# Kernel tuning notes

Hardware: AMD Instinct MI355X
Metric: run time of the kernel (lower is better)

## Reference

```python
import jax, jax.numpy as jnp
import numpy as np

DIM = 192
HEADS = 4
RED = 4  # DFRG reduction


def _conv1x1(x, w):
    # x: [b,c,h,w], w: [o,c] (1x1 conv, no bias)
    return jnp.einsum('bchw,oc->bohw', x, w)


def _dfrg(x, w_fc1, w_fc2, w_spatial):
    # channel gate (SE-style with avg+max pooling)
    avg = jnp.mean(x, axis=(2, 3), keepdims=True)          # [b,c,1,1]
    mx = jnp.max(x, axis=(2, 3), keepdims=True)            # [b,c,1,1]
    pool = jnp.concatenate([avg, mx], axis=1)              # [b,2c,1,1]
    sq = jax.nn.relu(_conv1x1(pool, w_fc1))                # [b,c/RED,1,1]
    channel_gate = jax.nn.sigmoid(_conv1x1(sq, w_fc2))     # [b,c,1,1]
    # spatial gate (7x7 conv over [mean_c, max_c])
    sp = jnp.concatenate([jnp.mean(x, axis=1, keepdims=True),
                          jnp.max(x, axis=1, keepdims=True)], axis=1)  # [b,2,h,w]
    sg = jax.lax.conv_general_dilated(
        sp, w_spatial, (1, 1), [(3, 3), (3, 3)],
        dimension_numbers=('NCHW', 'OIHW', 'NCHW'))
    spatial_gate = jax.nn.sigmoid(sg)                      # [b,1,h,w]
    return x * channel_gate * spatial_gate


def _forward(x, w_fc1, w_fc2, w_spatial, w_qkv, w_dw, w_proj, temperature):
    b, c, h, w = x.shape
    hd = c // HEADS
    x = _dfrg(x, w_fc1, w_fc2, w_spatial)
    # qkv 1x1 conv (out channels = 4c for elementwise gate) + depthwise 3x3
    qkv = _conv1x1(x, w_qkv)                               # [b,4c,h,w]
    qkv = jax.lax.conv_general_dilated(
        qkv, w_dw, (1, 1), [(1, 1), (1, 1)],
        dimension_numbers=('NCHW', 'OIHW', 'NCHW'),
        feature_group_count=4 * c)
    # channel order matches torch: [q (c), gate (c), k (c), v (c)]
    q, gate, k, v = jnp.split(qkv, [c, 2 * c, 3 * c], axis=1)
    heads = lambda t: t.reshape(b, HEADS, hd, h * w)       # b head c (h w)
    q, k, v, gate = heads(q), heads(k), heads(v), heads(gate)
    # L2-normalize over spatial axis (F.normalize, eps=1e-12)
    q = q / jnp.maximum(jnp.linalg.norm(q, axis=-1, keepdims=True), 1e-12)
    k = k / jnp.maximum(jnp.linalg.norm(k, axis=-1, keepdims=True), 1e-12)
    attn = jnp.einsum('bhcn,bhdn->bhcd', q, k) * temperature  # [b,H,hd,hd]
    attn = jax.nn.softmax(attn, axis=-1)
    out = jnp.einsum('bhcd,bhdn->bhcn', attn, v)
    out = out * jax.nn.sigmoid(gate)                       # elementwise gating
    out = out.reshape(b, c, h, w)
    return _conv1x1(out, w_proj)


def setup_inputs() -> dict:
    key = jax.random.key(0)
    ks = jax.random.split(key, 8)
    b, c, h, w = 8, DIM, 128, 128
    s = 0.02
    return {
        'x': jax.random.normal(ks[0], (b, c, h, w), jnp.float32),
        'w_fc1': jax.random.normal(ks[1], (c // RED, 2 * c), jnp.float32) * s,
        'w_fc2': jax.random.normal(ks[2], (c, c // RED), jnp.float32) * s,
        'w_spatial': jax.random.normal(ks[3], (1, 2, 7, 7), jnp.float32) * s,
        'w_qkv': jax.random.normal(ks[4], (4 * c, c), jnp.float32) * s,
        'w_dw': jax.random.normal(ks[5], (4 * c, 1, 3, 3), jnp.float32) * s,
        'w_proj': jax.random.normal(ks[6], (c, c), jnp.float32) * s,
        'temperature': jnp.ones((HEADS, 1, 1), jnp.float32),
    }


def reference(x, w_fc1, w_fc2, w_spatial, w_qkv, w_dw, w_proj, temperature):
    return _forward(x, w_fc1, w_fc2, w_spatial, w_qkv, w_dw, w_proj, temperature)
```

## Files before the change

### kernel.cpp

```cpp
#include <hip/hip_runtime.h>
#include <cstdint>
#include <type_traits>

typedef unsigned int u32;
typedef unsigned short u16;
typedef short v8s __attribute__((ext_vector_type(8)));
typedef float v4f __attribute__((ext_vector_type(4)));

#define B_ 8
#define C_ 192
#define HW_ 16384
#define C4_ 768

__device__ __forceinline__ float b2f(u16 u) {
  union { u32 i; float f; } v; v.i = ((u32)u) << 16; return v.f;
}
__device__ __forceinline__ u16 f2b(float f) {
  union { float f; u32 i; } v; v.f = f;
  u32 r = v.i + 0x7fffu + ((v.i >> 16) & 1u);
  return (u16)(r >> 16);
}
__device__ __forceinline__ void b2f2(u32 u, float& a, float& b) {
  union { u32 i; float f; } x, y;
  x.i = u << 16; y.i = u & 0xffff0000u;
  a = x.f; b = y.f;
}
__device__ __forceinline__ float lo16f(u32 u) {
  union { u32 i; float f; } x; x.i = u << 16; return x.f;
}
__device__ __forceinline__ float hi16f(u32 u) {
  union { u32 i; float f; } x; x.i = u & 0xffff0000u; return x.f;
}
__device__ __forceinline__ float sigm(float x) { return 1.f / (1.f + expf(-x)); }
__device__ __forceinline__ u32 pk2(u16 a, u16 b) { return (u32)a | ((u32)b << 16); }

__global__ __launch_bounds__(256) void k_f2b(const float* __restrict__ in, u16* __restrict__ out, int n) {
  int i = blockIdx.x * 256 + threadIdx.x;
  if (i < n) out[i] = f2b(in[i]);
}

__global__ __launch_bounds__(256) void k_channel_pool(const float* __restrict__ x,
                                                      float* __restrict__ avg, float* __restrict__ mx_) {
  int c = blockIdx.x, b = blockIdx.y, t = threadIdx.x;
  const float4* p = (const float4*)(x + (((size_t)b * C_ + c) << 14));
  float s = 0.f, m = -INFINITY;
  for (int i = t; i < 4096; i += 256) {
    float4 v = p[i];
    s += v.x + v.y + v.z + v.w;
    m = fmaxf(m, fmaxf(fmaxf(v.x, v.y), fmaxf(v.z, v.w)));
  }
  __shared__ float ss[256], sm[256];
  ss[t] = s; sm[t] = m; __syncthreads();
  for (int o = 128; o > 0; o >>= 1) {
    if (t < o) { ss[t] += ss[t + o]; sm[t] = fmaxf(sm[t], sm[t + o]); }
    __syncthreads();
  }
  if (t == 0) { avg[b * C_ + c] = ss[0] * (1.f / 16384.f); mx_[b * C_ + c] = sm[0]; }
}

__global__ __launch_bounds__(256) void k_channel_gate(const float* __restrict__ avg, const float* __restrict__ mx_,
                                                      const float* __restrict__ wfc1, const float* __restrict__ wfc2,
                                                      float* __restrict__ cgate) {
  int b = blockIdx.x, t = threadIdx.x;
  __shared__ float pool[384], sq[48];
  if (t < 192) { pool[t] = avg[b * C_ + t]; pool[192 + t] = mx_[b * C_ + t]; }
  __syncthreads();
  if (t < 48) {
    float s = 0.f;
    for (int k = 0; k < 384; ++k) s += wfc1[t * 384 + k] * pool[k];
    sq[t] = fmaxf(s, 0.f);
  }
  __syncthreads();
  if (t < 192) {
    float s = 0.f;
    for (int j = 0; j < 48; ++j) s += wfc2[t * 48 + j] * sq[j];
    cgate[b * C_ + t] = sigm(s);
  }
}

__global__ __launch_bounds__(256) void k_spatial_pool(const float* __restrict__ x, float* __restrict__ sp) {
  int b = blockIdx.y;
  int p4 = blockIdx.x * 256 + threadIdx.x;
  const float4* xb = (const float4*)(x + (((size_t)b * C_) << 14)) + p4;
  float4 s; s.x = s.y = s.z = s.w = 0.f;
  float4 m; m.x = m.y = m.z = m.w = -INFINITY;
#pragma unroll 4
  for (int c = 0; c < C_; ++c) {
    float4 v = xb[(size_t)c << 12];
    s.x += v.x; s.y += v.y; s.z += v.z; s.w += v.w;
    m.x = fmaxf(m.x, v.x); m.y = fmaxf(m.y, v.y);
    m.z = fmaxf(m.z, v.z); m.w = fmaxf(m.w, v.w);
  }
  float4 sm;
  sm.x = s.x * (1.f / 192.f); sm.y = s.y * (1.f / 192.f);
  sm.z = s.z * (1.f / 192.f); sm.w = s.w * (1.f / 192.f);
  *(float4*)(sp + (size_t)b * 32768 + p4 * 4) = sm;
  *(float4*)(sp + (size_t)b * 32768 + 16384 + p4 * 4) = m;
}

__global__ __launch_bounds__(256) void k_spatial_conv(const float* __restrict__ sp, const float* __restrict__ wsp,
                                                      float* __restrict__ sg) {
  int b = blockIdx.y;
  int p = blockIdx.x * 256 + threadIdx.x;
  int y = p >> 7, xx = p & 127;
  const float* s0 = sp + (size_t)b * 32768;
  float acc = 0.f;
  for (int ic = 0; ic < 2; ++ic)
    for (int ky = 0; ky < 7; ++ky) {
      int yy = y + ky - 3;
      if ((unsigned)yy >= 128u) continue;
      for (int kx = 0; kx < 7; ++kx) {
        int xp = xx + kx - 3;
        if ((unsigned)xp >= 128u) continue;
        acc += wsp[ic * 49 + ky * 7 + kx] * s0[ic * 16384 + yy * 128 + xp];
      }
    }
  sg[(size_t)b * 16384 + p] = sigm(acc);
}

__global__ __launch_bounds__(256) void k_gxT(const float* __restrict__ x, const float* __restrict__ cg,
                                             const float* __restrict__ sg, u16* __restrict__ gxT, int b0) {
  int zb = blockIdx.y, b = b0 + zb, t = threadIdx.x;
  int hw0 = blockIdx.x * 64;
  __shared__ alignas(16) u16 Ls[64][196];
  int l16 = t & 15, grp = t >> 4;
  int px0 = l16 * 4;
  float4 sg4 = *(const float4*)(sg + (size_t)b * 16384 + hw0 + px0);
#pragma unroll
  for (int it = 0; it < 12; ++it) {
    int c = it * 16 + grp;
    float cgv = cg[b * C_ + c];
    float4 v = *(const float4*)(x + (((size_t)b * C_ + c) << 14) + hw0 + px0);
    Ls[px0 + 0][c] = f2b(v.x * cgv * sg4.x);
    Ls[px0 + 1][c] = f2b(v.y * cgv * sg4.y);
    Ls[px0 + 2][c] = f2b(v.z * cgv * sg4.z);
    Ls[px0 + 3][c] = f2b(v.w * cgv * sg4.w);
  }
  __syncthreads();
  u32* out = (u32*)gxT;
  for (int r = 0; r < 24; ++r) {
    int ci = r * 256 + t;
    int row = ci / 96, col = ci - row * 96;
    u32 v = *(const u32*)&Ls[row][col * 2];
    out[((size_t)zb * HW_ + hw0 + row) * 96 + col] = v;
  }
}

template <int M, typename OutT>
__global__ __launch_bounds__(256) void gemm_bt(const u16* __restrict__ A, const u16* __restrict__ BT,
                                               OutT* __restrict__ C) {
  const int K = 192;
  int b = blockIdx.z;
  int n0 = blockIdx.x * 128, m0 = blockIdx.y * 128;
  const u16* Bb = BT + (size_t)b * HW_ * K;
  __shared__ alignas(16) u16 SMEM[2 * 128 * 104];
  u16 (*As)[104] = (u16(*)[104])SMEM;
  u16 (*Bs)[104] = (u16(*)[104])(SMEM + 128 * 104);
  int t = threadIdx.x;
  int wave = t >> 6, lane = t & 63, l16 = lane & 15, quad = lane >> 4;
  int wr = wave >> 1, wc = wave & 1;
  v4f acc[4][4] = {};
  for (int kc = 0; kc < K; kc += 64) {
#pragma unroll
    for (int r = 0; r < 4; ++r) {
      int ci = r * 256 + t;
      int row = ci >> 3, ks = (ci & 7) * 8;
      uint4 av; av.x = av.y = av.z = av.w = 0u;
      if (M >= 768 || m0 + row < M) av = *(const uint4*)(A + (size_t)(m0 + row) * K + kc + ks);
      *(uint4*)&As[row][ks] = av;
      uint4 bv = *(const uint4*)(Bb + (size_t)(n0 + row) * K + kc + ks);
      *(uint4*)&Bs[row][ks] = bv;
    }
    __syncthreads();
#pragma unroll
    for (int s = 0; s < 2; ++s) {
      v8s af[4], bf[4];
#pragma unroll
      for (int mt = 0; mt < 4; ++mt) af[mt] = *(const v8s*)&As[wr * 64 + mt * 16 + l16][s * 32 + quad * 8];
#pragma unroll
      for (int nt = 0; nt < 4; ++nt) bf[nt] = *(const v8s*)&Bs[wc * 64 + nt * 16 + l16][s * 32 + quad * 8];
#pragma unroll
      for (int mt = 0; mt < 4; ++mt)
#pragma unroll
        for (int nt = 0; nt < 4; ++nt)
          acc[mt][nt] = __builtin_amdgcn_mfma_f32_16x16x32_bf16(af[mt], bf[nt], acc[mt][nt], 0, 0, 0);
    }
    __syncthreads();
  }
  char* eb = (char*)SMEM + wave * 10240;
  if constexpr (std::is_same<OutT, u16>::value) {
#pragma unroll
    for (int mt = 0; mt < 4; ++mt)
#pragma unroll
      for (int nt = 0; nt < 4; ++nt)
#pragma unroll
        for (int r = 0; r < 4; ++r) {
          int rr = mt * 16 + quad * 4 + r;
          *(u16*)(eb + rr * 160 + (nt * 16 + l16) * 2) = f2b(acc[mt][nt][r]);
        }
#pragma unroll
    for (int it = 0; it < 8; ++it) {
      int rr = it * 8 + (lane >> 3);
      uint4 v = *(const uint4*)(eb + rr * 160 + (lane & 7) * 16);
      int gm = m0 + wr * 64 + rr;
      size_t off = ((size_t)b * M + gm) * (size_t)HW_ + n0 + wc * 64 + (lane & 7) * 8;
      *(uint4*)(C + off) = v;
    }
  } else {
#pragma unroll
    for (int half = 0; half < 2; ++half) {
#pragma unroll
      for (int mt = 0; mt < 2; ++mt)
#pragma unroll
        for (int nt = 0; nt < 4; ++nt)
#pragma unroll
          for (int r = 0; r < 4; ++r) {
            int rr = mt * 16 + quad * 4 + r;
            *(float*)(eb + rr * 272 + (nt * 16 + l16) * 4) = acc[half * 2 + mt][nt][r];
          }
#pragma unroll
      for (int it = 0; it < 8; ++it) {
        int rr = it * 4 + (lane >> 4);
        uint4 v = *(const uint4*)(eb + rr * 272 + (lane & 15) * 16);
        int gm = m0 + wr * 64 + half * 32 + rr;
        if (gm < M) {
          size_t off = ((size_t)b * M + gm) * (size_t)HW_ + n0 + wc * 64 + (lane & 15) * 4;
          *(uint4*)((float*)C + off) = v;
        }
      }
    }
  }
}

__global__ __launch_bounds__(256) void k_dw(const u16* __restrict__ in, const float* __restrict__ wdw,
                                            u16* __restrict__ out) {
  int oc = blockIdx.y;
  size_t base = ((size_t)(blockIdx.z * C4_ + oc)) << 14;
  int t = threadIdx.x;
  int rp = t >> 4;
  int xseg = t & 15;
  int y0 = blockIdx.x * 32 + rp * 2;
  int x0 = xseg * 8;
  const float* wd = wdw + oc * 9;
  float w0 = wd[0], w1 = wd[1], w2 = wd[2];
  float w3 = wd[3], w4 = wd[4], w5 = wd[5];
  float w6 = wd[6], w7 = wd[7], w8 = wd[8];

  float r[4][10];
#pragma unroll
  for (int ky = 0; ky < 4; ++ky) {
    int yy = y0 + ky - 1;
    uint4 v; v.x = v.y = v.z = v.w = 0u;
    if ((unsigned)yy < 128u) v = *(const uint4*)(in + base + ((size_t)yy << 7) + x0);
    b2f2(v.x, r[ky][1], r[ky][2]);
    b2f2(v.y, r[ky][3], r[ky][4]);
    b2f2(v.z, r[ky][5], r[ky][6]);
    b2f2(v.w, r[ky][7], r[ky][8]);
    u32 pw = (u32)__shfl_up((int)v.w, 1);
    u32 nx = (u32)__shfl_down((int)v.x, 1);
    r[ky][0] = (xseg == 0) ? 0.f : hi16f(pw);
    r[ky][9] = (xseg == 15) ? 0.f : lo16f(nx);
  }

#pragma unroll
  for (int oy = 0; oy < 2; ++oy) {
    float acc[8];
#pragma unroll
    for (int j = 0; j < 8; ++j) {
      acc[j] = w0 * r[oy][j]     + w1 * r[oy][j + 1]     + w2 * r[oy][j + 2]
             + w3 * r[oy + 1][j] + w4 * r[oy + 1][j + 1] + w5 * r[oy + 1][j + 2]
             + w6 * r[oy + 2][j] + w7 * r[oy + 2][j + 1] + w8 * r[oy + 2][j + 2];
    }
    uint4 o;
    o.x = pk2(f2b(acc[0]), f2b(acc[1]));
    o.y = pk2(f2b(acc[2]), f2b(acc[3]));
    o.z = pk2(f2b(acc[4]), f2b(acc[5]));
    o.w = pk2(f2b(acc[6]), f2b(acc[7]));
    *(uint4*)(out + base + (((size_t)(y0 + oy)) << 7) + x0) = o;
  }
}

__global__ __launch_bounds__(256) void k_rnorm(const u16* __restrict__ qkv, float* __restrict__ rqn,
                                               float* __restrict__ rkn, int b0) {
  int j = blockIdx.x, zb = blockIdx.y, b = b0 + zb, t = threadIdx.x;
  int ch = (j < 192) ? j : (384 + j - 192);
  const uint4* p = (const uint4*)(qkv + (((size_t)zb * C4_ + ch) << 14));
  float s = 0.f;
  for (int i = t; i < 2048; i += 256) {
    uint4 v = p[i];
    float a, c;
    b2f2(v.x, a, c); s += a * a + c * c;
    b2f2(v.y, a, c); s += a * a + c * c;
    b2f2(v.z, a, c); s += a * a + c * c;
    b2f2(v.w, a, c); s += a * a + c * c;
  }
  __shared__ float ss[256];
  ss[t] = s; __syncthreads();
  for (int o = 128; o > 0; o >>= 1) {
    if (t < o) ss[t] += ss[t + o];
    __syncthreads();
  }
  if (t == 0) {
    float r = 1.f / fmaxf(sqrtf(ss[0]), 1e-12f);
    if (j < 192) rqn[b * C_ + j] = r; else rkn[b * C_ + (j - 192)] = r;
  }
}

__global__ __launch_bounds__(256) void k_qk(const u16* __restrict__ qkv, float* __restrict__ Spart, int b0) {
  int split = blockIdx.x;
  int zb = blockIdx.y >> 2, h = blockIdx.y & 3;
  int bh = (b0 + zb) * 4 + h;
  int t = threadIdx.x, w = t >> 6, lane = t & 63, l16 = lane & 15, quad = lane >> 4;
  __shared__ union U {
    struct { alignas(16) u16 Qs[48][136]; alignas(16) u16 Ks[48][136]; } qk;
    float R[4][48][49];
  } Sh;
  const u16* qb = qkv + (((size_t)zb * C4_ + h * 48) << 14);
  const u16* kb = qkv + (((size_t)zb * C4_ + 384 + h * 48) << 14);
  v4f acc[3][3] = {};
  for (int chunk = 0; chunk < 8; ++chunk) {
    int nb = split * 1024 + chunk * 128;
#pragma unroll
    for (int r = 0; r < 3; ++r) {
      int ci = r * 256 + t;
      int row = ci >> 4, cs = (ci & 15) * 8;
      *(uint4*)&Sh.qk.Qs[row][cs] = *(const uint4*)(qb + ((size_t)row << 14) + nb + cs);
      *(uint4*)&Sh.qk.Ks[row][cs] = *(const uint4*)(kb + ((size_t)row << 14) + nb + cs);
    }
    __syncthreads();
    v8s qf[3], kf[3];
#pragma unroll
    for (int mt = 0; mt < 3; ++mt) qf[mt] = *(const v8s*)&Sh.qk.Qs[mt * 16 + l16][w * 32 + quad * 8];
#pragma unroll
    for (int nt = 0; nt < 3; ++nt) kf[nt] = *(const v8s*)&Sh.qk.Ks[nt * 16 + l16][w * 32 + quad * 8];
#pragma unroll
    for (int mt = 0; mt < 3; ++mt)
#pragma unroll
      for (int nt = 0; nt < 3; ++nt)
        acc[mt][nt] = __builtin_amdgcn_mfma_f32_16x16x32_bf16(qf[mt], kf[nt], acc[mt][nt], 0, 0, 0);
    __syncthreads();
  }
#pragma unroll
  for (int mt = 0; mt < 3; ++mt)
#pragma unroll
    for (int nt = 0; nt < 3; ++nt)
#pragma unroll
      for (int r = 0; r < 4; ++r)
        Sh.R[w][nt * 16 + l16][mt * 16 + quad * 4 + r] = acc[mt][nt][r];
  __syncthreads();
  float* out = Spart + ((size_t)split * 32 + bh) * 2304;
#pragma unroll
  for (int rr = 0; rr < 9; ++rr) {
    int e = rr * 256 + t;
    int c = e / 48, d = e - c * 48;
    out[e] = (Sh.R[0][d][c] + Sh.R[1][d][c]) + (Sh.R[2][d][c] + Sh.R[3][d][c]);
  }
}

__global__ __launch_bounds__(256) void k_softmax(const float* __restrict__ Spart, const float* __restrict__ rqn,
                                                 const float* __restrict__ rkn, const float* __restrict__ temp,
                                                 float* __restrict__ attn, int b0) {
  int bh = b0 * 4 + blockIdx.x;
  int b = bh >> 2, h = bh & 3, t = threadIdx.x;
  __shared__ float Sm[2304];
  float tv = temp[h];
  for (int r = 0; r < 9; ++r) {
    int e = r * 256 + t;
    float s = 0.f;
#pragma unroll
    for (int p = 0; p < 16; ++p) s += Spart[((size_t)p * 32 + bh) * 2304 + e];
    int c = e / 48, d = e - c * 48;
    Sm[e] = s * rqn[b * C_ + h * 48 + c] * rkn[b * C_ + h * 48 + d] * tv;
  }
  __syncthreads();
  if (t < 48) {
    float m = -INFINITY;
#pragma unroll
    for (int d = 0; d < 48; ++d) m = fmaxf(m, Sm[t * 48 + d]);
    float ex[48];
    float sum = 0.f;
#pragma unroll
    for (int d = 0; d < 48; ++d) { ex[d] = expf(Sm[t * 48 + d] - m); sum += ex[d]; }
    float inv = 1.f / sum;
#pragma unroll
    for (int d = 0; d < 48; ++d) attn[(size_t)bh * 2304 + t * 48 + d] = ex[d] * inv;
  }
}

__global__ __launch_bounds__(256) void k_av(const u16* __restrict__ qkv, const float* __restrict__ attn,
                                            u16* __restrict__ ogT, int b0) {
  int zb = blockIdx.y >> 2, h = blockIdx.y & 3;
  int bh = (b0 + zb) * 4 + h;
  int t = threadIdx.x;
  int n0 = blockIdx.x * 512;
  __shared__ alignas(16) u16 Vs[48][520];
  __shared__ alignas(16) float SlT[48][48];
  for (int r = 0; r < 9; ++r) {
    int e = r * 256 + t;
    int c = e / 48, d = e - c * 48;
    SlT[d][c] = attn[(size_t)bh * 2304 + e];
  }
  const u16* vb = qkv + (((size_t)zb * C4_ + 576 + h * 48) << 14);
  for (int r = 0; r < 12; ++r) {
    int ci = r * 256 + t;
    int row = ci >> 6, cs = (ci & 63) * 8;
    *(uint4*)&Vs[row][cs] = *(const uint4*)(vb + ((size_t)row << 14) + n0 + cs);
  }
  __syncthreads();
  int grp = t >> 6, nl = t & 63;
  int n = n0 + nl * 8;
  float acc[12][8] = {};
  for (int d = 0; d < 48; ++d) {
    uint4 vv = *(const uint4*)&Vs[d][nl * 8];
    float v[8];
    b2f2(vv.x, v[0], v[1]); b2f2(vv.y, v[2], v[3]);
    b2f2(vv.z, v[4], v[5]); b2f2(vv.w, v[6], v[7]);
    const float4* sr = (const float4*)&SlT[d][grp * 12];
    float4 sa = sr[0], sb = sr[1], sc = sr[2];
    float sv[12] = {sa.x, sa.y, sa.z, sa.w, sb.x, sb.y, sb.z, sb.w, sc.x, sc.y, sc.z, sc.w};
#pragma unroll
    for (int cc = 0; cc < 12; ++cc)
#pragma unroll
      for (int j = 0; j < 8; ++j) acc[cc][j] += sv[cc] * v[j];
  }
  const u16* gb = qkv + (((size_t)zb * C4_ + 192 + h * 48) << 14);
#pragma unroll
  for (int cc = 0; cc < 12; ++cc) {
    int c = grp * 12 + cc;
    uint4 g4 = *(const uint4*)(gb + ((size_t)c << 14) + n);
    float g[8];
    b2f2(g4.x, g[0], g[1]); b2f2(g4.y, g[2], g[3]);
    b2f2(g4.z, g[4], g[5]); b2f2(g4.w, g[6], g[7]);
#pragma unroll
    for (int j = 0; j < 8; ++j) acc[cc][j] *= sigm(g[j]);
  }
#pragma unroll
  for (int j = 0; j < 8; ++j) {
    u16 vals[12];
#pragma unroll
    for (int cc = 0; cc < 12; ++cc) vals[cc] = f2b(acc[cc][j]);
    u16* dst = ogT + ((size_t)zb * HW_ + n + j) * 192 + h * 48 + grp * 12;
    uint2* d2 = (uint2*)dst;
    uint2 w0, w1, w2;
    w0.x = pk2(vals[0], vals[1]);  w0.y = pk2(vals[2], vals[3]);
    w1.x = pk2(vals[4], vals[5]);  w1.y = pk2(vals[6], vals[7]);
    w2.x = pk2(vals[8], vals[9]);  w2.y = pk2(vals[10], vals[11]);
    d2[0] = w0; d2[1] = w1; d2[2] = w2;
  }
}

extern "C" void kernel_launch(void* const* d_in, const int* in_sizes, int n_in,
                              void* d_out, int out_size, void* d_ws, size_t ws_size,
                              hipStream_t stream) {
  const float* x     = (const float*)d_in[0];
  const float* wfc1  = (const float*)d_in[1];
  const float* wfc2  = (const float*)d_in[2];
  const float* wsp   = (const float*)d_in[3];
  const float* wqkv  = (const float*)d_in[4];
  const float* wdw   = (const float*)d_in[5];
  const float* wproj = (const float*)d_in[6];
  const float* temp  = (const float*)d_in[7];
  float* out = (float*)d_out;
  char* W = (char*)d_ws;

  constexpr size_t OFF_AVG   = 0;
  constexpr size_t OFF_MAX   = 8192;
  constexpr size_t OFF_CG    = 16384;
  constexpr size_t OFF_RQN   = 24576;
  constexpr size_t OFF_RKN   = 32768;
  constexpr size_t OFF_WQB   = 40960;
  constexpr size_t OFF_WPB   = OFF_WQB + 294912;
  constexpr size_t OFF_SP    = OFF_WPB + 73728;
  constexpr size_t OFF_SG    = OFF_SP + 1048576;
  constexpr size_t OFF_ATT   = OFF_SG + 524288;
  constexpr size_t OFF_SPART = OFF_ATT + 294912;
  constexpr size_t OFF_BIG   = OFF_SPART + 4718592;
  const size_t GXT_B = (size_t)HW_ * 192 * 2;
  const size_t QKV_B = (size_t)C4_ * HW_ * 2;

  float* avg   = (float*)(W + OFF_AVG);
  float* mx    = (float*)(W + OFF_MAX);
  float* cg    = (float*)(W + OFF_CG);
  float* rqn   = (float*)(W + OFF_RQN);
  float* rkn   = (float*)(W + OFF_RKN);
  u16*   wqb   = (u16*)(W + OFF_WQB);
  u16*   wpb   = (u16*)(W + OFF_WPB);
  float* sp    = (float*)(W + OFF_SP);
  float* sg    = (float*)(W + OFF_SG);
  float* attn  = (float*)(W + OFF_ATT);
  float* Spart = (float*)(W + OFF_SPART);

  int NB = 8;
  while (NB > 1 && (OFF_BIG + (size_t)NB * (GXT_B + 2 * QKV_B)) > ws_size) NB >>= 1;

  u16* gxT  = (u16*)(W + OFF_BIG);
  u16* qkvr = (u16*)(W + OFF_BIG + (size_t)NB * GXT_B);
  u16* qkvd = (u16*)(W + OFF_BIG + (size_t)NB * (GXT_B + QKV_B));
  u16* ogT  = qkvr;

  k_f2b<<<(147456 + 255) / 256, 256, 0, stream>>>(wqkv, wqb, 147456);
  k_f2b<<<(36864 + 255) / 256, 256, 0, stream>>>(wproj, wpb, 36864);
  k_channel_pool<<<dim3(C_, B_), 256, 0, stream>>>(x, avg, mx);
  k_channel_gate<<<B_, 256, 0, stream>>>(avg, mx, wfc1, wfc2, cg);
  k_spatial_pool<<<dim3(16, B_), 256, 0, stream>>>(x, sp);
  k_spatial_conv<<<dim3(64, B_), 256, 0, stream>>>(sp, wsp, sg);

  for (int b0 = 0; b0 < B_; b0 += NB) {
    k_gxT<<<dim3(256, NB), 256, 0, stream>>>(x, cg, sg, gxT, b0);
    gemm_bt<768, u16><<<dim3(128, 6, NB), 256, 0, stream>>>(wqb, gxT, qkvr);
    k_dw<<<dim3(4, C4_, NB), 256, 0, stream>>>(qkvr, wdw, qkvd);
    k_rnorm<<<dim3(384, NB), 256, 0, stream>>>(qkvd, rqn, rkn, b0);
    k_qk<<<dim3(16, NB * 4), 256, 0, stream>>>(qkvd, Spart, b0);
    k_softmax<<<NB * 4, 256, 0, stream>>>(Spart, rqn, rkn, temp, attn, b0);
    k_av<<<dim3(32, NB * 4), 256, 0, stream>>>(qkvd, attn, ogT, b0);
    gemm_bt<192, float><<<dim3(128, 2, NB), 256, 0, stream>>>(wpb, ogT, out + (size_t)b0 * C_ * HW_);
  }
}
```

Baseline: 578.6 us.

## Fuse q/k L2-norm reduction into depthwise conv and widen GEMM K-chunk

The depthwise 3x3 kernel now loads a whole 128x128 channel plane into LDS per block, computes 8 output rows per thread with a rolling row buffer, and accumulates the sum of squares of the bf16-rounded outputs for q and k channels. This removes the separate k_rnorm pass, which re-read q and k from global memory. Separately, the bf16 GEMM now loads K in chunks of 96 instead of 64, so it runs two K iterations and fewer barriers. The cost is 32KB of LDS per dw block, which may lower occupancy, plus an integer divide by 12 in the GEMM load index.

```diff
diff --git a/kernel.cpp b/kernel.cpp
--- a/kernel.cpp
+++ b/kernel.cpp
@@ -24,12 +24,6 @@
   union { u32 i; float f; } x, y;
   x.i = u << 16; y.i = u & 0xffff0000u;
   a = x.f; b = y.f;
-}
-__device__ __forceinline__ float lo16f(u32 u) {
-  union { u32 i; float f; } x; x.i = u << 16; return x.f;
-}
-__device__ __forceinline__ float hi16f(u32 u) {
-  union { u32 i; float f; } x; x.i = u & 0xffff0000u; return x.f;
 }
 __device__ __forceinline__ float sigm(float x) { return 1.f / (1.f + expf(-x)); }
 __device__ __forceinline__ u32 pk2(u16 a, u16 b) { return (u32)a | ((u32)b << 16); }
@@ -160,11 +154,11 @@
   int wave = t >> 6, lane = t & 63, l16 = lane & 15, quad = lane >> 4;
   int wr = wave >> 1, wc = wave & 1;
   v4f acc[4][4] = {};
-  for (int kc = 0; kc < K; kc += 64) {
-#pragma unroll
-    for (int r = 0; r < 4; ++r) {
+  for (int kc = 0; kc < K; kc += 96) {
+#pragma unroll
+    for (int r = 0; r < 6; ++r) {
       int ci = r * 256 + t;
-      int row = ci >> 3, ks = (ci & 7) * 8;
+      int row = ci / 12, ks = (ci - row * 12) * 8;
       uint4 av; av.x = av.y = av.z = av.w = 0u;
       if (M >= 768 || m0 + row < M) av = *(const uint4*)(A + (size_t)(m0 + row) * K + kc + ks);
       *(uint4*)&As[row][ks] = av;
@@ -173,7 +167,7 @@
     }
     __syncthreads();
 #pragma unroll
-    for (int s = 0; s < 2; ++s) {
+    for (int s = 0; s < 3; ++s) {
       v8s af[4], bf[4];
 #pragma unroll
       for (int mt = 0; mt < 4; ++mt) af[mt] = *(const v8s*)&As[wr * 64 + mt * 16 + l16][s * 32 + quad * 8];
@@ -233,76 +227,81 @@
 }
 
 __global__ __launch_bounds__(256) void k_dw(const u16* __restrict__ in, const float* __restrict__ wdw,
-                                            u16* __restrict__ out) {
-  int oc = blockIdx.y;
-  size_t base = ((size_t)(blockIdx.z * C4_ + oc)) << 14;
+                                            u16* __restrict__ out, float* __restrict__ rqn,
+                                            float* __restrict__ rkn, int b0) {
+  int oc = blockIdx.x, zb = blockIdx.y;
+  size_t base = ((size_t)(zb * C4_ + oc)) << 14;
   int t = threadIdx.x;
-  int rp = t >> 4;
-  int xseg = t & 15;
-  int y0 = blockIdx.x * 32 + rp * 2;
-  int x0 = xseg * 8;
+  __shared__ alignas(16) u16 Ls[128][128];
+  __shared__ float red[256];
+  const uint4* gin = (const uint4*)(in + base);
+#pragma unroll
+  for (int r = 0; r < 8; ++r) {
+    int ci = r * 256 + t;
+    *(uint4*)&Ls[ci >> 4][(ci & 15) << 3] = gin[ci];
+  }
+  __syncthreads();
   const float* wd = wdw + oc * 9;
   float w0 = wd[0], w1 = wd[1], w2 = wd[2];
   float w3 = wd[3], w4 = wd[4], w5 = wd[5];
   float w6 = wd[6], w7 = wd[7], w8 = wd[8];
-
-  float r[4][10];
-#pragma unroll
-  for (int ky = 0; ky < 4; ++ky) {
-    int yy = y0 + ky - 1;
-    uint4 v; v.x = v.y = v.z = v.w = 0u;
-    if ((unsigned)yy < 128u) v = *(const uint4*)(in + base + ((size_t)yy << 7) + x0);
-    b2f2(v.x, r[ky][1], r[ky][2]);
-    b2f2(v.y, r[ky][3], r[ky][4]);
-    b2f2(v.z, r[ky][5], r[ky][6]);
-    b2f2(v.w, r[ky][7], r[ky][8]);
-    u32 pw = (u32)__shfl_up((int)v.w, 1);
-    u32 nx = (u32)__shfl_down((int)v.x, 1);
-    r[ky][0] = (xseg == 0) ? 0.f : hi16f(pw);
-    r[ky][9] = (xseg == 15) ? 0.f : lo16f(nx);
-  }
-
-#pragma unroll
-  for (int oy = 0; oy < 2; ++oy) {
+  int x0 = (t & 15) << 3;
+  int ybase = (t >> 4) << 3;
+
+  float rw[3][10];
+  auto ldrow = [&](int yy, float* d) {
+    if ((unsigned)yy < 128u) {
+      uint4 v = *(const uint4*)&Ls[yy][x0];
+      b2f2(v.x, d[1], d[2]); b2f2(v.y, d[3], d[4]);
+      b2f2(v.z, d[5], d[6]); b2f2(v.w, d[7], d[8]);
+      d[0] = (x0 == 0) ? 0.f : b2f(Ls[yy][x0 - 1]);
+      d[9] = (x0 == 120) ? 0.f : b2f(Ls[yy][x0 + 8]);
+    } else {
+#pragma unroll
+      for (int j = 0; j < 10; ++j) d[j] = 0.f;
+    }
+  };
+  ldrow(ybase - 1, rw[0]);
+  ldrow(ybase,     rw[1]);
+  bool isq = (oc < 192), isk = (oc >= 384 && oc < 576);
+  float ssq = 0.f;
+#pragma unroll
+  for (int oy = 0; oy < 8; ++oy) {
+    ldrow(ybase + oy + 1, rw[(oy + 2) % 3]);
+    const float* ra = rw[oy % 3];
+    const float* rb = rw[(oy + 1) % 3];
+    const float* rc = rw[(oy + 2) % 3];
     float acc[8];
 #pragma unroll
     for (int j = 0; j < 8; ++j) {
-      acc[j] = w0 * r[oy][j]     + w1 * r[oy][j + 1]     + w2 * r[oy][j + 2]
-             + w3 * r[oy + 1][j] + w4 * r[oy + 1][j + 1] + w5 * r[oy + 1][j + 2]
-             + w6 * r[oy + 2][j] + w7 * r[oy + 2][j + 1] + w8 * r[oy + 2][j + 2];
-    }
+      acc[j] = w0 * ra[j] + w1 * ra[j + 1] + w2 * ra[j + 2]
+             + w3 * rb[j] + w4 * rb[j + 1] + w5 * rb[j + 2]
+             + w6 * rc[j] + w7 * rc[j + 1] + w8 * rc[j + 2];
+    }
+    u16 vb[8];
+#pragma unroll
+    for (int j = 0; j < 8; ++j) vb[j] = f2b(acc[j]);
     uint4 o;
-    o.x = pk2(f2b(acc[0]), f2b(acc[1]));
-    o.y = pk2(f2b(acc[2]), f2b(acc[3]));
-    o.z = pk2(f2b(acc[4]), f2b(acc[5]));
-    o.w = pk2(f2b(acc[6]), f2b(acc[7]));
-    *(uint4*)(out + base + (((size_t)(y0 + oy)) << 7) + x0) = o;
-  }
-}
-
-__global__ __launch_bounds__(256) void k_rnorm(const u16* __restrict__ qkv, float* __restrict__ rqn,
-                                               float* __restrict__ rkn, int b0) {
-  int j = blockIdx.x, zb = blockIdx.y, b = b0 + zb, t = threadIdx.x;
-  int ch = (j < 192) ? j : (384 + j - 192);
-  const uint4* p = (const uint4*)(qkv + (((size_t)zb * C4_ + ch) << 14));
-  float s = 0.f;
-  for (int i = t; i < 2048; i += 256) {
-    uint4 v = p[i];
-    float a, c;
-    b2f2(v.x, a, c); s += a * a + c * c;
-    b2f2(v.y, a, c); s += a * a + c * c;
-    b2f2(v.z, a, c); s += a * a + c * c;
-    b2f2(v.w, a, c); s += a * a + c * c;
-  }
-  __shared__ float ss[256];
-  ss[t] = s; __syncthreads();
-  for (int o = 128; o > 0; o >>= 1) {
-    if (t < o) ss[t] += ss[t + o];
+    o.x = pk2(vb[0], vb[1]); o.y = pk2(vb[2], vb[3]);
+    o.z = pk2(vb[4], vb[5]); o.w = pk2(vb[6], vb[7]);
+    *(uint4*)(out + base + (((size_t)(ybase + oy)) << 7) + x0) = o;
+    if (isq || isk) {
+#pragma unroll
+      for (int j = 0; j < 8; ++j) { float f = b2f(vb[j]); ssq += f * f; }
+    }
+  }
+  if (isq || isk) {
+    red[t] = ssq;
     __syncthreads();
-  }
-  if (t == 0) {
-    float r = 1.f / fmaxf(sqrtf(ss[0]), 1e-12f);
-    if (j < 192) rqn[b * C_ + j] = r; else rkn[b * C_ + (j - 192)] = r;
+    for (int o2 = 128; o2 > 0; o2 >>= 1) {
+      if (t < o2) red[t] += red[t + o2];
+      __syncthreads();
+    }
+    if (t == 0) {
+      float r = 1.f / fmaxf(sqrtf(red[0]), 1e-12f);
+      int b = b0 + zb;
+      if (isq) rqn[b * C_ + oc] = r; else rkn[b * C_ + (oc - 384)] = r;
+    }
   }
 }
 
@@ -508,8 +507,7 @@
   for (int b0 = 0; b0 < B_; b0 += NB) {
     k_gxT<<<dim3(256, NB), 256, 0, stream>>>(x, cg, sg, gxT, b0);
     gemm_bt<768, u16><<<dim3(128, 6, NB), 256, 0, stream>>>(wqb, gxT, qkvr);
-    k_dw<<<dim3(4, C4_, NB), 256, 0, stream>>>(qkvr, wdw, qkvd);
-    k_rnorm<<<dim3(384, NB), 256, 0, stream>>>(qkvd, rqn, rkn, b0);
+    k_dw<<<dim3(C4_, NB), 256, 0, stream>>>(qkvr, wdw, qkvd, rqn, rkn, b0);
     k_qk<<<dim3(16, NB * 4), 256, 0, stream>>>(qkvd, Spart, b0);
     k_softmax<<<NB * 4, 256, 0, stream>>>(Spart, rqn, rkn, temp, attn, b0);
     k_av<<<dim3(32, NB * 4), 256, 0, stream>>>(qkvd, attn, ogT, b0);
```

New measurement: 567.7 us. Within noise of the previous version (-1.9%).
